# Performance work log

Measured on AMD Instinct MI355X. Metric: run time of the kernel, lower is better.

Reference implementation:

```python
import jax, jax.numpy as jnp
import numpy as np
from jax import lax

T = 8  # primary_vec_length


def setup_inputs() -> dict:
    key = jax.random.key(0)
    k1, k2, k3 = jax.random.split(key, 3)
    x = jax.random.normal(k1, (32, 256, 64, 64), dtype=jnp.float32)
    # Conv2d weight [out_ch, in_ch, kH, kW], kaiming-ish scale
    W = jax.random.normal(k2, (32, 256, 9, 9), dtype=jnp.float32) * 0.01
    b = jax.random.normal(k3, (32,), dtype=jnp.float32) * 0.01
    return {"x": x, "W": W, "b": b}


def reference(x, W, b):
    B = x.shape[0]
    # Conv2d(kernel=9, stride=2, valid). The original applies this conv T times
    # to identical stacked copies of x; compute it once and broadcast (same math).
    conv = lax.conv_general_dilated(
        x, W, window_strides=(2, 2), padding="VALID",
        dimension_numbers=("NCHW", "OIHW", "NCHW"))
    conv = conv + b[None, :, None, None]            # [B, C, H', W']
    s = jnp.broadcast_to(conv[:, None], (B, T) + conv.shape[1:])  # [B, T, C, H', W']
    # squash along dim=1 (the capsule-vector / time dim)
    sq = jnp.sum(s * s, axis=1, keepdims=True)      # [B, 1, C, H', W']
    scale = sq / (1.0 + sq) / jnp.sqrt(sq + 1e-8)
    squ = s * scale                                  # [B, T, C, H', W']
    squ = squ.reshape(B, T, -1)                      # [B, T, C*H'*W']
    squ = jnp.transpose(squ, (0, 2, 1))[..., None]   # [B, N, T, 1]
    return squ
```

## Files before the change

### kernel.cpp

```cpp
#include <hip/hip_runtime.h>
#include <hip/hip_bf16.h>
#include <stdint.h>

typedef _Float16 f16;
typedef _Float16 f16x8 __attribute__((ext_vector_type(8)));
typedef float f32x16 __attribute__((ext_vector_type(16)));
typedef float f32x4 __attribute__((ext_vector_type(4)));
typedef uint32_t u32x4 __attribute__((ext_vector_type(4)));
typedef uint32_t u32x2 __attribute__((ext_vector_type(2)));

#define GLL16(gp, lp)                                                          \
  __builtin_amdgcn_global_load_lds(                                            \
      (const __attribute__((address_space(1))) void*)(gp),                     \
      (__attribute__((address_space(3))) void*)(lp), 16, 0, 0)

#define WAITCNT_VM(N)                                                          \
  __builtin_amdgcn_s_waitcnt(((N)&0xF) | ((((N) >> 4) & 3) << 14) | 0x0F70)

__global__ __launch_bounds__(256) void nchw_to_nhwc_f16(
    const float* __restrict__ x, f16* __restrict__ xt) {
  __shared__ __align__(16) uint32_t tile[64 * 128];
  const int bh = blockIdx.x;
  const int t = threadIdx.x;
  const float* src = x + (size_t)(bh >> 6) * (256 * 4096) + (bh & 63) * 64;

  const int w4 = t & 15;
  const int cq = t >> 4;
  const int xorv = 4 * (w4 & 7);
#pragma unroll
  for (int it = 0; it < 4; ++it) {
    const int c0 = it * 64 + cq * 4;
    float4 v0 = *(const float4*)(src + (size_t)(c0 + 0) * 4096 + w4 * 4);
    float4 v1 = *(const float4*)(src + (size_t)(c0 + 1) * 4096 + w4 * 4);
    float4 v2 = *(const float4*)(src + (size_t)(c0 + 2) * 4096 + w4 * 4);
    float4 v3 = *(const float4*)(src + (size_t)(c0 + 3) * 4096 + w4 * 4);
    const float* p0 = (const float*)&v0;
    const float* p1 = (const float*)&v1;
    const float* p2 = (const float*)&v2;
    const float* p3 = (const float*)&v3;
    const int u = it * 32 + cq * 2;
#pragma unroll
    for (int jw = 0; jw < 4; ++jw) {
      const int w = w4 * 4 + jw;
      f16 h0 = (f16)p0[jw], h1 = (f16)p1[jw], h2 = (f16)p2[jw], h3 = (f16)p3[jw];
      uint32_t lo = (uint32_t)__builtin_bit_cast(uint16_t, h0) |
                    ((uint32_t)__builtin_bit_cast(uint16_t, h1) << 16);
      uint32_t hi = (uint32_t)__builtin_bit_cast(uint16_t, h2) |
                    ((uint32_t)__builtin_bit_cast(uint16_t, h3) << 16);
      u32x2 pk = {lo, hi};
      *(u32x2*)&tile[w * 128 + (u ^ xorv)] = pk;
    }
  }
  __syncthreads();
  f16* dst = xt + (size_t)bh * 16384;
#pragma unroll
  for (int it = 0; it < 8; ++it) {
    const int idx = it * 256 + t;
    const int w = idx >> 5;
    const int g = idx & 31;
    const u32x4 v = *(const u32x4*)&tile[w * 128 + ((g * 4) ^ (4 * ((w >> 2) & 7)))];
    *(u32x4*)(dst + idx * 8) = v;
  }
}

__global__ __launch_bounds__(256) void pack_w(const float* __restrict__ W,
                                              f16* __restrict__ wt) {
  __shared__ float lds[10368];
  const int t = threadIdx.x;
  const int co = blockIdx.x >> 1;
  const int cih = blockIdx.x & 1;
  const float* src = W + (size_t)(co * 256 + cih * 128) * 81;
  for (int i = t; i < 10368; i += 256) lds[i] = src[i];
  __syncthreads();
  for (int j = t; j < 1296; j += 256) {
    const int kk = j >> 4;
    const int t16 = j & 15;
    const int cicl = t16 >> 2;
    const int ci8 = (t16 & 3) * 8;
    f16 tmp[8];
#pragma unroll
    for (int e = 0; e < 8; ++e)
      tmp[e] = (f16)lds[(cicl * 32 + ci8 + e) * 81 + kk];
    *(f16x8*)&wt[(size_t)kk * 8192 + (cih * 4 + cicl) * 1024 + co * 32 + ci8] =
        *(f16x8*)tmp;
  }
}

__global__ __launch_bounds__(256, 5) void conv_direct(
    const f16* __restrict__ xt, const f16* __restrict__ wt,
    float* __restrict__ convp) {
  __shared__ __align__(16) char smem[32768];
  const int tid = threadIdx.x;
  const int lane = tid & 63;
  const int wave = tid >> 6;
  const int hh = lane >> 5;

  const int blk = blockIdx.x;
  const int xcd = blk & 7;
  const int r = blk >> 3;
  const int i4 = r / 56;
  const int rr = r - i4 * 56;
  const int bimg = xcd * 4 + i4;
  const int oh = rr >> 1;
  const int cih = rr & 1;
  const int cic = cih * 4 + wave;

  const char* xtb = (const char*)xt;
  const char* wtb = (const char*)wt;
  char* lws = smem + wave * 8192;

  const int w_l = lane >> 2;
  const int u_l = w_l >> 1;
  const int gbase = ((w_l ^ (u_l & 1)) * 512) + (((lane & 3) ^ (u_l & 3)) * 16);

  auto stage = [&](int kh, int par) {
    const int h = 2 * oh + kh;
    const char* base = xtb + (size_t)((bimg * 4096 + h * 64) * 512 + cic * 64 + gbase);
    char* lb = lws + par * 4096;
    GLL16(base, lb);
    GLL16(base + 8192, lb + 1024);
    GLL16(base + 16384, lb + 2048);
    GLL16(base + 24576, lb + 3072);
  };

  const int m = lane & 31;
  int offA[9];
#pragma unroll
  for (int kw = 0; kw < 9; ++kw) {
    int w = 2 * m + kw;
    if (w > 63) w = 63;
    const int u = w >> 1;
    offA[kw] = ((w ^ (u & 1)) * 64) + ((hh ^ (u & 3)) * 16);
  }

  const int bl = m * 64 + hh * 16 + cic * 2048;
  auto bload = [&](int kk, int s) -> f16x8 {
    return *(const f16x8*)(wtb + kk * 16384 + bl + s * 32);
  };

  f32x16 acc;
#pragma unroll
  for (int i = 0; i < 16; ++i) acc[i] = 0.f;

#define KW_ISSUE(KW, WC, KKN)                                                  \
  {                                                                            \
    const f16x8 bm0 = bload((KKN), 0);                                         \
    const f16x8 bm1 = bload((KKN), 1);                                         \
    WAITCNT_VM(WC);                                                            \
    __builtin_amdgcn_sched_barrier(0);                                         \
    const f16x8 a0 = *(const f16x8*)(lb + offA[KW]);                           \
    acc = __builtin_amdgcn_mfma_f32_32x32x16_f16(a0, bc0, acc, 0, 0, 0);       \
    const f16x8 a1 = *(const f16x8*)(lb + (offA[KW] ^ 32));                    \
    acc = __builtin_amdgcn_mfma_f32_32x32x16_f16(a1, bc1, acc, 0, 0, 0);       \
    bc0 = bn0; bc1 = bn1; bn0 = bm0; bn1 = bm1;                                \
  }
#define KW_NOISSUE(KW, WC)                                                     \
  {                                                                            \
    WAITCNT_VM(WC);                                                            \
    __builtin_amdgcn_sched_barrier(0);                                         \
    const f16x8 a0 = *(const f16x8*)(lb + offA[KW]);                           \
    acc = __builtin_amdgcn_mfma_f32_32x32x16_f16(a0, bc0, acc, 0, 0, 0);       \
    const f16x8 a1 = *(const f16x8*)(lb + (offA[KW] ^ 32));                    \
    acc = __builtin_amdgcn_mfma_f32_32x32x16_f16(a1, bc1, acc, 0, 0, 0);       \
    bc0 = bn0; bc1 = bn1;                                                      \
  }

  stage(0, 0);
  f16x8 bc0 = bload(0, 0), bc1 = bload(0, 1);
  f16x8 bn0 = bload(1, 0), bn1 = bload(1, 1);
  stage(1, 1);

  for (int kh = 0; kh < 8; ++kh) {
    const char* lb = lws + (kh & 1) * 4096;
    const int kkb = kh * 9;
    KW_ISSUE(0, 8, kkb + 2)
    KW_ISSUE(1, 8, kkb + 3)
    KW_ISSUE(2, 4, kkb + 4)
    KW_ISSUE(3, 4, kkb + 5)
    KW_ISSUE(4, 4, kkb + 6)
    KW_ISSUE(5, 4, kkb + 7)
    KW_ISSUE(6, 4, kkb + 8)
    KW_ISSUE(7, 4, kkb + 9)
    KW_ISSUE(8, 4, kkb + 10)
    if (kh < 7) stage(kh + 2, kh & 1);
  }
  {
    const char* lb = lws;
    KW_ISSUE(0, 4, 74)
    KW_ISSUE(1, 4, 75)
    KW_ISSUE(2, 4, 76)
    KW_ISSUE(3, 4, 77)
    KW_ISSUE(4, 4, 78)
    KW_ISSUE(5, 4, 79)
    KW_ISSUE(6, 4, 80)
    KW_NOISSUE(7, 2)
    KW_NOISSUE(8, 0)
  }
#undef KW_ISSUE
#undef KW_NOISSUE

  __syncthreads();
  float* red = (float*)smem;
#pragma unroll
  for (int rI = 0; rI < 16; ++rI) {
    const int row = (rI & 3) + 8 * (rI >> 2) + 4 * hh;
    red[(wave * 32 + row) * 33 + m] = acc[rI];
  }
  __syncthreads();
  const int mm = tid >> 3;
  const int c0 = (tid & 7) * 4;
  if (mm < 28) {
    float s0 = 0.f, s1 = 0.f, s2 = 0.f, s3 = 0.f;
#pragma unroll
    for (int w = 0; w < 4; ++w) {
      const float* rp = red + (w * 32 + mm) * 33 + c0;
      s0 += rp[0]; s1 += rp[1]; s2 += rp[2]; s3 += rp[3];
    }
    const f32x4 o4 = {s0, s1, s2, s3};
    const int p = bimg * 784 + oh * 28 + mm;
    *(f32x4*)&convp[(size_t)cih * 802816 + (size_t)p * 32 + c0] = o4;
  }
}

__global__ __launch_bounds__(256) void epilogue(const float* __restrict__ convp,
                                                const float* __restrict__ bias,
                                                float* __restrict__ out) {
  const int gi = blockIdx.x * 256 + threadIdx.x;
  const int base = gi * 8;
  const int p = gi >> 2;
  const int co0 = (gi & 3) * 8;
  const int bi = p / 784;
  const int pix = p - bi * 784;
  f32x4 v0 = {0.f, 0.f, 0.f, 0.f}, v1 = {0.f, 0.f, 0.f, 0.f};
#pragma unroll
  for (int qq = 0; qq < 2; ++qq) {
    v0 += *(const f32x4*)&convp[(size_t)qq * 802816 + base];
    v1 += *(const f32x4*)&convp[(size_t)qq * 802816 + base + 4];
  }
  float vb[8];
#pragma unroll
  for (int jj = 0; jj < 4; ++jj) {
    vb[jj] = v0[jj] + bias[co0 + jj];
    vb[4 + jj] = v1[jj] + bias[co0 + 4 + jj];
  }
  float* ob = out + (size_t)bi * 200704 + pix * 8;
#pragma unroll
  for (int jj = 0; jj < 8; ++jj) {
    const float vv = vb[jj];
    const float sq = 8.f * vv * vv;
    const float scale = sq / ((1.f + sq) * sqrtf(sq + 1e-8f));
    const float y = vv * scale;
    const f32x4 qv = {y, y, y, y};
    float* o = ob + (size_t)(co0 + jj) * 6272;
    *(f32x4*)o = qv;
    *(f32x4*)(o + 4) = qv;
  }
}

extern "C" void kernel_launch(void* const* d_in, const int* in_sizes, int n_in,
                              void* d_out, int out_size, void* d_ws,
                              size_t ws_size, hipStream_t stream) {
  const float* x = (const float*)d_in[0];
  const float* W = (const float*)d_in[1];
  const float* bias = (const float*)d_in[2];
  float* out = (float*)d_out;

  char* ws = (char*)d_ws;
  f16* xt = (f16*)ws;
  f16* wt = (f16*)(ws + 67108864);
  float* convp = (float*)(ws + 67108864 + 1327104);

  nchw_to_nhwc_f16<<<dim3(2048), dim3(256), 0, stream>>>(x, xt);
  pack_w<<<dim3(64), dim3(256), 0, stream>>>(W, wt);
  conv_direct<<<dim3(1792), dim3(256), 0, stream>>>(xt, wt, convp);
  epilogue<<<dim3(392), dim3(256), 0, stream>>>(convp, bias, out);
}
```

Measured before the change: 302.3 us.

## Compute two output rows per block, loading A fragments directly from global

The conv kernel now computes two adjacent output rows per block with two accumulators. Each loaded input row feeds both output rows: kernel-row j for one and j-2 for the other. This halves the input-row traffic per output and the block count. The LDS staging through global_load_lds is replaced by direct global vector loads with a 3-deep register prefetch. To make those loads coalesced, the input transpose and the weight packing are reordered into even/odd-column and subgroup-friendly layouts. Occupancy drops, since launch bounds go from 5 to 3 blocks, and register pressure rises with double accumulators and prefetch buffers.

```diff
diff --git a/kernel.cpp b/kernel.cpp
--- a/kernel.cpp
+++ b/kernel.cpp
@@ -9,13 +9,7 @@
 typedef uint32_t u32x4 __attribute__((ext_vector_type(4)));
 typedef uint32_t u32x2 __attribute__((ext_vector_type(2)));
 
-#define GLL16(gp, lp)                                                          \
-  __builtin_amdgcn_global_load_lds(                                            \
-      (const __attribute__((address_space(1))) void*)(gp),                     \
-      (__attribute__((address_space(3))) void*)(lp), 16, 0, 0)
-
-#define WAITCNT_VM(N)                                                          \
-  __builtin_amdgcn_s_waitcnt(((N)&0xF) | ((((N) >> 4) & 3) << 14) | 0x0F70)
+#define MFMA(A, B, C) __builtin_amdgcn_mfma_f32_32x32x16_f16((A), (B), (C), 0, 0, 0)
 
 __global__ __launch_bounds__(256) void nchw_to_nhwc_f16(
     const float* __restrict__ x, f16* __restrict__ xt) {
@@ -41,25 +35,27 @@
     const int u = it * 32 + cq * 2;
 #pragma unroll
     for (int jw = 0; jw < 4; ++jw) {
-      const int w = w4 * 4 + jw;
       f16 h0 = (f16)p0[jw], h1 = (f16)p1[jw], h2 = (f16)p2[jw], h3 = (f16)p3[jw];
       uint32_t lo = (uint32_t)__builtin_bit_cast(uint16_t, h0) |
                     ((uint32_t)__builtin_bit_cast(uint16_t, h1) << 16);
       uint32_t hi = (uint32_t)__builtin_bit_cast(uint16_t, h2) |
                     ((uint32_t)__builtin_bit_cast(uint16_t, h3) << 16);
       u32x2 pk = {lo, hi};
+      const int w = w4 * 4 + jw;
       *(u32x2*)&tile[w * 128 + (u ^ xorv)] = pk;
     }
   }
   __syncthreads();
-  f16* dst = xt + (size_t)bh * 16384;
+  f16* dstb = xt + (size_t)bh * 16384;
 #pragma unroll
   for (int it = 0; it < 8; ++it) {
-    const int idx = it * 256 + t;
-    const int w = idx >> 5;
-    const int g = idx & 31;
-    const u32x4 v = *(const u32x4*)&tile[w * 128 + ((g * 4) ^ (4 * ((w >> 2) & 7)))];
-    *(u32x4*)(dst + idx * 8) = v;
+    const int n = it * 256 + t;
+    const int w2 = n & 31;
+    const int par = (n >> 5) & 1;
+    const int g8 = n >> 6;
+    const int w = par + 2 * w2;
+    const u32x4 v = *(const u32x4*)&tile[w * 128 + ((g8 * 4) ^ (4 * ((w >> 2) & 7)))];
+    *(u32x4*)(dstb + n * 8) = v;
   }
 }
 
@@ -76,149 +72,119 @@
     const int kk = j >> 4;
     const int t16 = j & 15;
     const int cicl = t16 >> 2;
-    const int ci8 = (t16 & 3) * 8;
+    const int sg = t16 & 3;
+    const int cin = ((sg >> 1) & 1) * 16 + (sg & 1) * 8;
     f16 tmp[8];
 #pragma unroll
     for (int e = 0; e < 8; ++e)
-      tmp[e] = (f16)lds[(cicl * 32 + ci8 + e) * 81 + kk];
-    *(f16x8*)&wt[(size_t)kk * 8192 + (cih * 4 + cicl) * 1024 + co * 32 + ci8] =
-        *(f16x8*)tmp;
-  }
-}
-
-__global__ __launch_bounds__(256, 5) void conv_direct(
+      tmp[e] = (f16)lds[(cicl * 32 + cin + e) * 81 + kk];
+    const int cic = cih * 4 + cicl;
+    *(f16x8*)&wt[(size_t)(((kk * 8 + cic) * 4 + sg) * 32 + co) * 8] = *(f16x8*)tmp;
+  }
+}
+
+__global__ __launch_bounds__(256, 3) void conv_direct(
     const f16* __restrict__ xt, const f16* __restrict__ wt,
     float* __restrict__ convp) {
-  __shared__ __align__(16) char smem[32768];
+  __shared__ float red[4 * 32 * 33];
   const int tid = threadIdx.x;
   const int lane = tid & 63;
   const int wave = tid >> 6;
+  const int m = lane & 31;
   const int hh = lane >> 5;
 
   const int blk = blockIdx.x;
   const int xcd = blk & 7;
   const int r = blk >> 3;
-  const int i4 = r / 56;
-  const int rr = r - i4 * 56;
+  const int i4 = r / 28;
+  const int rr = r - i4 * 28;
   const int bimg = xcd * 4 + i4;
-  const int oh = rr >> 1;
+  const int ohp = rr >> 1;
   const int cih = rr & 1;
   const int cic = cih * 4 + wave;
 
-  const char* xtb = (const char*)xt;
-  const char* wtb = (const char*)wt;
-  char* lws = smem + wave * 8192;
-
-  const int w_l = lane >> 2;
-  const int u_l = w_l >> 1;
-  const int gbase = ((w_l ^ (u_l & 1)) * 512) + (((lane & 3) ^ (u_l & 3)) * 16);
-
-  auto stage = [&](int kh, int par) {
-    const int h = 2 * oh + kh;
-    const char* base = xtb + (size_t)((bimg * 4096 + h * 64) * 512 + cic * 64 + gbase);
-    char* lb = lws + par * 4096;
-    GLL16(base, lb);
-    GLL16(base + 8192, lb + 1024);
-    GLL16(base + 16384, lb + 2048);
-    GLL16(base + 24576, lb + 3072);
-  };
-
-  const int m = lane & 31;
-  int offA[9];
-#pragma unroll
-  for (int kw = 0; kw < 9; ++kw) {
-    int w = 2 * m + kw;
-    if (w > 63) w = 63;
-    const int u = w >> 1;
-    offA[kw] = ((w ^ (u & 1)) * 64) + ((hh ^ (u & 3)) * 16);
-  }
-
-  const int bl = m * 64 + hh * 16 + cic * 2048;
-  auto bload = [&](int kk, int s) -> f16x8 {
-    return *(const f16x8*)(wtb + kk * 16384 + bl + s * 32);
-  };
-
-  f32x16 acc;
-#pragma unroll
-  for (int i = 0; i < 16; ++i) acc[i] = 0.f;
-
-#define KW_ISSUE(KW, WC, KKN)                                                  \
+  const char* xb = (const char*)xt;
+  const char* wb = (const char*)wt;
+
+  const char* ab = xb + ((size_t)(bimg * 64 + 4 * ohp) * 32768 +
+                         cic * 4096 + hh * 1024 + m * 16);
+  const int boff = cic * 2048 + hh * 512 + m * 16;
+
+#define ALOAD(AB, KW, P) \
+  (*(const f16x8*)((AB) + (P) * 2048 + ((KW)&1) * 512 + ((KW) >> 1) * 16))
+#define BLOAD(KK, S) \
+  (*(const f16x8*)(wb + (size_t)(KK) * 16384 + (S) * 1024 + boff))
+
+  f32x16 acc0, acc1;
+#pragma unroll
+  for (int i = 0; i < 16; ++i) { acc0[i] = 0.f; acc1[i] = 0.f; }
+
+#define SLAB_BODY(T0A, T1A, KKB0, KKB1)                                        \
   {                                                                            \
-    const f16x8 bm0 = bload((KKN), 0);                                         \
-    const f16x8 bm1 = bload((KKN), 1);                                         \
-    WAITCNT_VM(WC);                                                            \
-    __builtin_amdgcn_sched_barrier(0);                                         \
-    const f16x8 a0 = *(const f16x8*)(lb + offA[KW]);                           \
-    acc = __builtin_amdgcn_mfma_f32_32x32x16_f16(a0, bc0, acc, 0, 0, 0);       \
-    const f16x8 a1 = *(const f16x8*)(lb + (offA[KW] ^ 32));                    \
-    acc = __builtin_amdgcn_mfma_f32_32x32x16_f16(a1, bc1, acc, 0, 0, 0);       \
-    bc0 = bn0; bc1 = bn1; bn0 = bm0; bn1 = bm1;                                \
-  }
-#define KW_NOISSUE(KW, WC)                                                     \
-  {                                                                            \
-    WAITCNT_VM(WC);                                                            \
-    __builtin_amdgcn_sched_barrier(0);                                         \
-    const f16x8 a0 = *(const f16x8*)(lb + offA[KW]);                           \
-    acc = __builtin_amdgcn_mfma_f32_32x32x16_f16(a0, bc0, acc, 0, 0, 0);       \
-    const f16x8 a1 = *(const f16x8*)(lb + (offA[KW] ^ 32));                    \
-    acc = __builtin_amdgcn_mfma_f32_32x32x16_f16(a1, bc1, acc, 0, 0, 0);       \
-    bc0 = bn0; bc1 = bn1;                                                      \
-  }
-
-  stage(0, 0);
-  f16x8 bc0 = bload(0, 0), bc1 = bload(0, 1);
-  f16x8 bn0 = bload(1, 0), bn1 = bload(1, 1);
-  stage(1, 1);
-
-  for (int kh = 0; kh < 8; ++kh) {
-    const char* lb = lws + (kh & 1) * 4096;
-    const int kkb = kh * 9;
-    KW_ISSUE(0, 8, kkb + 2)
-    KW_ISSUE(1, 8, kkb + 3)
-    KW_ISSUE(2, 4, kkb + 4)
-    KW_ISSUE(3, 4, kkb + 5)
-    KW_ISSUE(4, 4, kkb + 6)
-    KW_ISSUE(5, 4, kkb + 7)
-    KW_ISSUE(6, 4, kkb + 8)
-    KW_ISSUE(7, 4, kkb + 9)
-    KW_ISSUE(8, 4, kkb + 10)
-    if (kh < 7) stage(kh + 2, kh & 1);
-  }
-  {
-    const char* lb = lws;
-    KW_ISSUE(0, 4, 74)
-    KW_ISSUE(1, 4, 75)
-    KW_ISSUE(2, 4, 76)
-    KW_ISSUE(3, 4, 77)
-    KW_ISSUE(4, 4, 78)
-    KW_ISSUE(5, 4, 79)
-    KW_ISSUE(6, 4, 80)
-    KW_NOISSUE(7, 2)
-    KW_NOISSUE(8, 0)
-  }
-#undef KW_ISSUE
-#undef KW_NOISSUE
-
-  __syncthreads();
-  float* red = (float*)smem;
-#pragma unroll
-  for (int rI = 0; rI < 16; ++rI) {
-    const int row = (rI & 3) + 8 * (rI >> 2) + 4 * hh;
-    red[(wave * 32 + row) * 33 + m] = acc[rI];
-  }
-  __syncthreads();
+    f16x8 a0[3], a1[3], b00[3], b01[3], b10[3], b11[3];                        \
+    _Pragma("unroll") for (int k = 0; k < 3; ++k) {                            \
+      a0[k] = ALOAD(ab, k, 0);                                                 \
+      a1[k] = ALOAD(ab, k, 1);                                                 \
+      if (T0A) { b00[k] = BLOAD((KKB0) + k, 0); b01[k] = BLOAD((KKB0) + k, 1); } \
+      if (T1A) { b10[k] = BLOAD((KKB1) + k, 0); b11[k] = BLOAD((KKB1) + k, 1); } \
+    }                                                                          \
+    _Pragma("unroll") for (int kw = 0; kw < 9; ++kw) {                         \
+      const int sl = kw % 3;                                                   \
+      const f16x8 ca0 = a0[sl], ca1 = a1[sl];                                  \
+      f16x8 t00, t01, t10, t11;                                                \
+      if (T0A) { t00 = b00[sl]; t01 = b01[sl]; }                               \
+      if (T1A) { t10 = b10[sl]; t11 = b11[sl]; }                               \
+      if (kw + 3 < 9) {                                                        \
+        a0[sl] = ALOAD(ab, kw + 3, 0);                                         \
+        a1[sl] = ALOAD(ab, kw + 3, 1);                                         \
+        if (T0A) { b00[sl] = BLOAD((KKB0) + kw + 3, 0);                        \
+                   b01[sl] = BLOAD((KKB0) + kw + 3, 1); }                      \
+        if (T1A) { b10[sl] = BLOAD((KKB1) + kw + 3, 0);                        \
+                   b11[sl] = BLOAD((KKB1) + kw + 3, 1); }                      \
+      }                                                                        \
+      if (T0A) { acc0 = MFMA(ca0, t00, acc0); acc0 = MFMA(ca1, t01, acc0); }   \
+      if (T1A) { acc1 = MFMA(ca0, t10, acc1); acc1 = MFMA(ca1, t11, acc1); }   \
+    }                                                                          \
+  }
+
+  for (int j = 0; j < 2; ++j) {
+    SLAB_BODY(1, 0, j * 9, 0)
+    ab += 32768;
+  }
+  for (int j = 2; j < 9; ++j) {
+    SLAB_BODY(1, 1, j * 9, (j - 2) * 9)
+    ab += 32768;
+  }
+  for (int j = 9; j < 11; ++j) {
+    SLAB_BODY(0, 1, 0, (j - 2) * 9)
+    ab += 32768;
+  }
+#undef SLAB_BODY
+#undef ALOAD
+#undef BLOAD
+
   const int mm = tid >> 3;
   const int c0 = (tid & 7) * 4;
-  if (mm < 28) {
-    float s0 = 0.f, s1 = 0.f, s2 = 0.f, s3 = 0.f;
-#pragma unroll
-    for (int w = 0; w < 4; ++w) {
-      const float* rp = red + (w * 32 + mm) * 33 + c0;
-      s0 += rp[0]; s1 += rp[1]; s2 += rp[2]; s3 += rp[3];
+#pragma unroll
+  for (int half = 0; half < 2; ++half) {
+    __syncthreads();
+#pragma unroll
+    for (int rI = 0; rI < 16; ++rI) {
+      const int row = (rI & 3) + 8 * (rI >> 2) + 4 * hh;
+      red[(wave * 32 + row) * 33 + m] = half ? acc1[rI] : acc0[rI];
     }
-    const f32x4 o4 = {s0, s1, s2, s3};
-    const int p = bimg * 784 + oh * 28 + mm;
-    *(f32x4*)&convp[(size_t)cih * 802816 + (size_t)p * 32 + c0] = o4;
+    __syncthreads();
+    if (mm < 28) {
+      float s0 = 0.f, s1 = 0.f, s2 = 0.f, s3 = 0.f;
+#pragma unroll
+      for (int w = 0; w < 4; ++w) {
+        const float* rp = red + (w * 32 + mm) * 33 + c0;
+        s0 += rp[0]; s1 += rp[1]; s2 += rp[2]; s3 += rp[3];
+      }
+      const f32x4 o4 = {s0, s1, s2, s3};
+      const int p = bimg * 784 + (2 * ohp + half) * 28 + mm;
+      *(f32x4*)&convp[(size_t)cih * 802816 + (size_t)p * 32 + c0] = o4;
+    }
   }
 }
 
@@ -272,6 +238,6 @@
 
   nchw_to_nhwc_f16<<<dim3(2048), dim3(256), 0, stream>>>(x, xt);
   pack_w<<<dim3(64), dim3(256), 0, stream>>>(W, wt);
-  conv_direct<<<dim3(1792), dim3(256), 0, stream>>>(xt, wt, convp);
+  conv_direct<<<dim3(896), dim3(256), 0, stream>>>(xt, wt, convp);
   epilogue<<<dim3(392), dim3(256), 0, stream>>>(convp, bias, out);
 }
```

Result: faster. 295.3 us (-2.3%).
